# Kernel tuning notes

Hardware: AMD Instinct MI355X
Metric: run time of the kernel (lower is better)

## Reference

```python
import jax, jax.numpy as jnp
import numpy as np

B = 64; PAST = 128; FUTURE = 64; HID = 64; HEADS = 4
F = 16 + 8 + 24 + 3  # out_preprocess = 51


def _pre(cat, num, emb0, emb1, emb2):
    # pre_processing: embedding lookups per categorical column + last 3 float cols
    return jnp.concatenate([emb0[cat[:, 0]], emb1[cat[:, 1]], emb2[cat[:, 2]], num], axis=-1)


def _gat_conv(x, edge_index, lin_w, att_src, att_dst, bias, heads, out_ch):
    # PyG GATConv: concat=False (head mean), add_self_loops=True, leaky_relu slope 0.2
    N = x.shape[0]
    loops = jnp.arange(N, dtype=edge_index.dtype)
    src = jnp.concatenate([edge_index[0], loops])
    dst = jnp.concatenate([edge_index[1], loops])
    h = (x @ lin_w).reshape(N, heads, out_ch)          # [N, H, C]
    a_src = (h * att_src).sum(-1)                      # [N, H]
    a_dst = (h * att_dst).sum(-1)
    e = jax.nn.leaky_relu(a_src[src] + a_dst[dst], 0.2)  # [E, H]
    m = jax.lax.stop_gradient(jax.ops.segment_max(e, dst, num_segments=N))
    ex = jnp.exp(e - m[dst])
    s = jax.ops.segment_sum(ex, dst, num_segments=N)
    alpha = ex / (s[dst] + 1e-16)                      # softmax over in-edges per node
    out = jax.ops.segment_sum(alpha[:, :, None] * h[src], dst, num_segments=N)
    return out.mean(1) + bias                          # concat=False -> mean over heads


def setup_inputs() -> dict:
    ks = jax.random.split(jax.random.key(0), 17)
    N1, N2 = B * PAST, B * FUTURE
    E1, E2 = N1 * 16, N2 * 16
    return dict(
        cat1=jax.random.randint(ks[0], (N1, 3), 0, 7),
        num1=jax.random.normal(ks[1], (N1, 3), dtype=jnp.float32),
        cat2=jax.random.randint(ks[2], (N2, 3), 0, 7),
        num2=jax.random.normal(ks[3], (N2, 3), dtype=jnp.float32),
        e1=jax.random.randint(ks[4], (2, E1), 0, N1),
        e2=jax.random.randint(ks[5], (2, E2), 0, N2),
        A=jax.random.randint(ks[6], (PAST + FUTURE, PAST + FUTURE), 0, 2),
        emb0=0.1 * jax.random.normal(ks[7], (24, 16), dtype=jnp.float32),
        emb1=0.1 * jax.random.normal(ks[8], (7, 8), dtype=jnp.float32),
        emb2=0.1 * jax.random.normal(ks[9], (500, 24), dtype=jnp.float32),
        g1_lin=0.1 * jax.random.normal(ks[10], (F, HEADS * (F - 1)), dtype=jnp.float32),
        g1_asrc=0.1 * jax.random.normal(ks[11], (HEADS, F - 1), dtype=jnp.float32),
        g1_adst=0.1 * jax.random.normal(ks[12], (HEADS, F - 1), dtype=jnp.float32),
        g1_b=jnp.zeros((F - 1,), dtype=jnp.float32),
        g2_lin=0.1 * jax.random.normal(ks[13], (F, HEADS), dtype=jnp.float32),
        g2_asrc=0.1 * jax.random.normal(ks[14], (HEADS, 1), dtype=jnp.float32),
        g2_adst=0.1 * jax.random.normal(ks[15], (HEADS, 1), dtype=jnp.float32),
        g2_b=jnp.zeros((1,), dtype=jnp.float32),
        W=0.1 * jax.random.normal(ks[16], (F - 1, HID), dtype=jnp.float32),
    )


def reference(cat1, num1, cat2, num2, e1, e2, A, emb0, emb1, emb2,
              g1_lin, g1_asrc, g1_adst, g1_b, g2_lin, g2_asrc, g2_adst, g2_b, W):
    x = _pre(cat1, num1, emb0, emb1, emb2)                       # [B*PAST, F]
    x2 = _pre(cat2, num2, emb0, emb1, emb2).reshape(B, FUTURE, F)
    x1 = _gat_conv(x, e1, g1_lin, g1_asrc, g1_adst, g1_b, HEADS, F - 1).reshape(B, PAST, F - 1)
    # pairwise diff between every (future, past) node pair within a graph
    diff = x1[:, None, :, :] - x2[:, :, None, :F - 1]            # [B, FUTURE, PAST, F-1]
    M = W @ W.T
    M = M + M.T                                                  # WW^T + (WW^T)^T
    # original builds full [PAST, PAST] quadratic form and extracts diagonal;
    # compute only the diagonal: -0.5 * diff_i M diff_i
    alpha = -0.5 * jnp.einsum('bfpd,de,bfpe->bfp', diff, M, diff)
    mask = A[:PAST, PAST:].T                                     # [FUTURE, PAST]
    alpha = jnp.where(mask == 0, -jnp.inf, alpha)
    alpha = jax.nn.softmax(alpha, axis=-1)
    y_past = x.reshape(B, PAST, F)[:, :, -1:]                    # [B, PAST, 1]
    tmp = alpha @ y_past                                         # [B, FUTURE, 1]
    x2b = jnp.concatenate([x2[:, :, :F - 1], tmp], axis=-1)
    out = _gat_conv(x2b.reshape(-1, F), e2, g2_lin, g2_asrc, g2_adst, g2_b, HEADS, 1)
    return out.reshape(B, FUTURE)
```

## Files before the change

kernel.cpp:

```cpp
#include <hip/hip_runtime.h>

static constexpr int B_ = 64, PAST = 128, FUTURE = 64, F_ = 51;
static constexpr int N1 = B_ * PAST;
static constexpr int N2 = B_ * FUTURE;
static constexpr int E1 = N1 * 16;
static constexpr int E2 = N2 * 16;
static constexpr int MAXDEG = 64;
static constexpr int PB = 512;
static constexpr int FB = 256;
static constexpr int XITEMS = E1 + N1 + E2 + N2 + FUTURE * PAST;
static constexpr int XB = XITEMS / 256;
static constexpr int POISON_I = (int)0xAAAAAAAA;

__device__ __forceinline__ int depoison(int v) {
    int d = v - POISON_I;
    return (d >= 0 && d < 1000000) ? d : v;
}

__device__ __forceinline__
float node_feat(const int* cat, const float* num, const float* e0, const float* e1,
                const float* e2, int n, int t) {
    if (t < 16) return e0[cat[n * 3 + 0] * 16 + t];
    if (t < 24) return e1[cat[n * 3 + 1] * 8 + (t - 16)];
    if (t < 48) return e2[cat[n * 3 + 2] * 24 + (t - 24)];
    return num[n * 3 + (t - 48)];
}

__global__ __launch_bounds__(256) void k_all(
        const int* __restrict__ cat1, const float* __restrict__ num1,
        const int* __restrict__ cat2, const float* __restrict__ num2,
        const int* __restrict__ e1, const int* __restrict__ e2,
        const int* __restrict__ A,
        const float* __restrict__ emb0, const float* __restrict__ emb1,
        const float* __restrict__ emb2,
        const float* __restrict__ g1_lin, const float* __restrict__ g1_asrc,
        const float* __restrict__ g1_adst, const float* __restrict__ W,
        float* __restrict__ h1, float* __restrict__ asrc1, float* __restrict__ adst1,
        float* __restrict__ y1, float* __restrict__ x2g, float* __restrict__ P2,
        int* __restrict__ count1, int* __restrict__ slot1,
        int* __restrict__ count2, int* __restrict__ slot2,
        int* __restrict__ maskT) {
    __shared__ float L[10704];
    int blk = blockIdx.x, t = threadIdx.x;
    int lane = t & 63, wv = t >> 6;

    if (blk < PB) {
        float* Lg = L;
        float* Lx = L + 10200;
        float* redS = L + 10252;
        float* redD = L + 10452;
        for (int i = t; i < 10200; i += 256) Lg[i] = g1_lin[i];
        int n0 = blk * 16;
        for (int ni = 0; ni < 16; ++ni) {
            int n = n0 + ni;
            __syncthreads();
            if (t < F_) {
                float xv = node_feat(cat1, num1, emb0, emb1, emb2, n, t);
                Lx[t] = xv;
                if (t == 50) y1[n] = xv;
            }
            __syncthreads();
            if (t < 200) {
                float acc = 0.f;
                #pragma unroll
                for (int j = 0; j < F_; ++j) acc += Lx[j] * Lg[j * 200 + t];
                h1[n * 200 + t] = acc;
                redS[t] = acc * g1_asrc[t];
                redD[t] = acc * g1_adst[t];
            }
            __syncthreads();
            float s = (lane < 50) ? redS[wv * 50 + lane] : 0.f;
            float d = (lane < 50) ? redD[wv * 50 + lane] : 0.f;
            #pragma unroll
            for (int m = 32; m >= 1; m >>= 1) {
                s += __shfl_xor(s, m);
                d += __shfl_xor(d, m);
            }
            if (lane == 0) {
                asrc1[n * 4 + wv] = s;
                adst1[n * 4 + wv] = d;
            }
        }
        return;
    }

    if (blk < PB + FB) {
        float* Lw = L;
        float* Lx = L + 3200;
        for (int i = t; i < 3200; i += 256) Lw[i] = W[i];
        int n0 = (blk - PB) * 16;
        for (int r = 0; r < 4; ++r) {
            __syncthreads();
            if (t < 204) {
                int which = t / 51, j = t - which * 51;
                int n = n0 + r * 4 + which;
                float xv = node_feat(cat2, num2, emb0, emb1, emb2, n, j);
                Lx[which * 51 + j] = xv;
                x2g[n * F_ + j] = xv;
            }
            __syncthreads();
            int sub = t >> 6, k = t & 63;
            int n = n0 + r * 4 + sub;
            float acc = 0.f;
            #pragma unroll
            for (int j = 0; j < 50; ++j) acc += Lx[sub * 51 + j] * Lw[j * 64 + k];
            P2[n * 64 + k] = acc;
        }
        return;
    }

    int i = (blk - PB - FB) * 256 + t;
    if (i < E1) {
        int src = e1[i], dst = e1[E1 + i];
        int pos = depoison(atomicAdd(&count1[dst], 1));
        if (pos < MAXDEG) slot1[dst * MAXDEG + pos] = src;
    } else if (i < E1 + N1) {
        int n = i - E1;
        int pos = depoison(atomicAdd(&count1[n], 1));
        if (pos < MAXDEG) slot1[n * MAXDEG + pos] = n;
    } else if (i < E1 + N1 + E2) {
        int k = i - E1 - N1;
        int src = e2[k], dst = e2[E2 + k];
        int pos = depoison(atomicAdd(&count2[dst], 1));
        if (pos < MAXDEG) slot2[dst * MAXDEG + pos] = src;
    } else if (i < E1 + N1 + E2 + N2) {
        int n = i - E1 - N1 - E2;
        int pos = depoison(atomicAdd(&count2[n], 1));
        if (pos < MAXDEG) slot2[n * MAXDEG + pos] = n;
    } else {
        int k = i - (E1 + N1 + E2 + N2);
        int f = k >> 7, pp = k & 127;
        maskT[k] = A[pp * 192 + PAST + f];
    }
}

__global__ __launch_bounds__(256) void k_gat1(
        const int* __restrict__ count1, const int* __restrict__ slot1,
        const float* __restrict__ h1, const float* __restrict__ asrc1,
        const float* __restrict__ adst1, const float* __restrict__ g1_b,
        const float* __restrict__ W, float* __restrict__ P1) {
    __shared__ int   Ssrc[4][64];
    __shared__ float Sw[4][4][64];
    __shared__ float Sx[4][64];
    int t = threadIdx.x, lane = t & 63, wv = t >> 6;
    int n = (blockIdx.x * 256 + t) >> 6;
    int deg = min(depoison(count1[n]), MAXDEG);
    int my_src = (lane < deg) ? slot1[n * MAXDEG + lane] : 0;
    float ad0 = adst1[n * 4 + 0], ad1 = adst1[n * 4 + 1];
    float ad2 = adst1[n * 4 + 2], ad3 = adst1[n * 4 + 3];
    float ex0 = 0.f, ex1 = 0.f, ex2 = 0.f, ex3 = 0.f;
    if (lane < deg) {
        float e0 = asrc1[my_src * 4 + 0] + ad0;
        float e1 = asrc1[my_src * 4 + 1] + ad1;
        float e2 = asrc1[my_src * 4 + 2] + ad2;
        float e3 = asrc1[my_src * 4 + 3] + ad3;
        e0 = e0 >= 0.f ? e0 : 0.2f * e0;  ex0 = __expf(e0);
        e1 = e1 >= 0.f ? e1 : 0.2f * e1;  ex1 = __expf(e1);
        e2 = e2 >= 0.f ? e2 : 0.2f * e2;  ex2 = __expf(e2);
        e3 = e3 >= 0.f ? e3 : 0.2f * e3;  ex3 = __expf(e3);
    }
    float s0 = ex0, s1 = ex1, s2 = ex2, s3 = ex3;
    #pragma unroll
    for (int m = 32; m >= 1; m >>= 1) {
        s0 += __shfl_xor(s0, m);
        s1 += __shfl_xor(s1, m);
        s2 += __shfl_xor(s2, m);
        s3 += __shfl_xor(s3, m);
    }
    Ssrc[wv][lane] = my_src;
    Sw[wv][0][lane] = ex0 / (s0 + 1e-16f);
    Sw[wv][1][lane] = ex1 / (s1 + 1e-16f);
    Sw[wv][2][lane] = ex2 / (s2 + 1e-16f);
    Sw[wv][3][lane] = ex3 / (s3 + 1e-16f);
    __syncthreads();
    float acc0 = 0.f, acc1 = 0.f, acc2 = 0.f, acc3 = 0.f;
    for (int i = 0; i < deg; ++i) {
        int srci = Ssrc[wv][i];
        float w0 = Sw[wv][0][i], w1 = Sw[wv][1][i];
        float w2 = Sw[wv][2][i], w3 = Sw[wv][3][i];
        if (lane < 50) {
            const float* hr = &h1[srci * 200];
            acc0 += w0 * hr[lane];
            acc1 += w1 * hr[50 + lane];
            acc2 += w2 * hr[100 + lane];
            acc3 += w3 * hr[150 + lane];
        }
    }
    if (lane < 50)
        Sx[wv][lane] = 0.25f * (acc0 + acc1 + acc2 + acc3) + g1_b[lane];
    __syncthreads();
    float a = 0.f;
    #pragma unroll
    for (int j = 0; j < 50; ++j) a += Sx[wv][j] * W[j * 64 + lane];
    P1[n * 64 + lane] = a;
}

__global__ __launch_bounds__(256) void k_attn(
        const float* __restrict__ P1, const float* __restrict__ P2,
        const int* __restrict__ maskT, const float* __restrict__ y1,
        const float* __restrict__ x2g, const float* __restrict__ g2_lin,
        float* __restrict__ h2g) {
    __shared__ float P1s[64 * 129];
    __shared__ float ys[128];
    int b = blockIdx.x >> 2, fg = blockIdx.x & 3;
    int t = threadIdx.x, lane = t & 63, wv = t >> 6;
    const float* P1b = P1 + b * 8192;
    for (int i = t; i < 8192; i += 256) {
        int pp = i >> 6, kk = i & 63;
        P1s[kk * 129 + pp] = P1b[i];
    }
    if (t < 128) ys[t] = y1[b * 128 + t];
    __syncthreads();
    for (int j = 0; j < 4; ++j) {
        int f = fg * 16 + wv * 4 + j;
        int q = b * 64 + f;
        float p2k = P2[q * 64 + lane];
        float d2a = 0.f, d2b = 0.f;
        for (int k = 0; k < 64; ++k) {
            float bk = __shfl(p2k, k);
            float va = P1s[k * 129 + lane] - bk;
            float vb = P1s[k * 129 + 64 + lane] - bk;
            d2a += va * va;
            d2b += vb * vb;
        }
        int ma = maskT[f * 128 + lane];
        int mb = maskT[f * 128 + 64 + lane];
        float va = ma ? -d2a : -1e30f;
        float vb = mb ? -d2b : -1e30f;
        float mx = fmaxf(va, vb);
        #pragma unroll
        for (int m = 32; m >= 1; m >>= 1) mx = fmaxf(mx, __shfl_xor(mx, m));
        float wa = ma ? __expf(va - mx) : 0.f;
        float wb = mb ? __expf(vb - mx) : 0.f;
        float sw = wa + wb;
        float sy = wa * ys[lane] + wb * ys[64 + lane];
        #pragma unroll
        for (int m = 32; m >= 1; m >>= 1) {
            sw += __shfl_xor(sw, m);
            sy += __shfl_xor(sy, m);
        }
        float tsh = sy / sw;
        float xv = (lane < 50) ? x2g[q * F_ + lane] : 0.f;
        #pragma unroll
        for (int h = 0; h < 4; ++h) {
            float c = xv * g2_lin[lane * 4 + h];
            #pragma unroll
            for (int m = 32; m >= 1; m >>= 1) c += __shfl_xor(c, m);
            c += tsh * g2_lin[50 * 4 + h];
            if (lane == h) h2g[q * 4 + h] = c;
        }
    }
}

__global__ __launch_bounds__(256) void k_gat2(
        const int* __restrict__ count2, const int* __restrict__ slot2,
        const float* __restrict__ h2g, const float* __restrict__ g2_asrc,
        const float* __restrict__ g2_adst, const float* __restrict__ g2_b,
        float* __restrict__ out) {
    int wave = (blockIdx.x * blockDim.x + threadIdx.x) >> 6;
    int lane = threadIdx.x & 63;
    if (wave >= N2) return;
    int n = wave;
    int deg = min(depoison(count2[n]), MAXDEG);
    int my_src = (lane < deg) ? slot2[n * MAXDEG + lane] : 0;
    float ex[4], nm[4], adterm[4], as[4];
    #pragma unroll
    for (int h = 0; h < 4; ++h) {
        as[h] = g2_asrc[h];
        adterm[h] = h2g[n * 4 + h] * g2_adst[h];
        ex[h] = 0.f; nm[h] = 0.f;
    }
    if (lane < deg) {
        #pragma unroll
        for (int h = 0; h < 4; ++h) {
            float hs = h2g[my_src * 4 + h];
            float e = hs * as[h] + adterm[h];
            e = e >= 0.f ? e : 0.2f * e;
            float xv = __expf(e);
            ex[h] = xv;
            nm[h] = xv * hs;
        }
    }
    #pragma unroll
    for (int m = 32; m >= 1; m >>= 1) {
        #pragma unroll
        for (int h = 0; h < 4; ++h) {
            ex[h] += __shfl_xor(ex[h], m);
            nm[h] += __shfl_xor(nm[h], m);
        }
    }
    if (lane == 0) {
        float o = 0.f;
        #pragma unroll
        for (int h = 0; h < 4; ++h) o += nm[h] / (ex[h] + 1e-16f);
        out[n] = 0.25f * o + g2_b[0];
    }
}

extern "C" void kernel_launch(void* const* d_in, const int* in_sizes, int n_in,
                              void* d_out, int out_size, void* d_ws, size_t ws_size,
                              hipStream_t stream) {
    const int*   cat1    = (const int*)  d_in[0];
    const float* num1    = (const float*)d_in[1];
    const int*   cat2    = (const int*)  d_in[2];
    const float* num2    = (const float*)d_in[3];
    const int*   e1      = (const int*)  d_in[4];
    const int*   e2      = (const int*)  d_in[5];
    const int*   A       = (const int*)  d_in[6];
    const float* emb0    = (const float*)d_in[7];
    const float* emb1    = (const float*)d_in[8];
    const float* emb2    = (const float*)d_in[9];
    const float* g1_lin  = (const float*)d_in[10];
    const float* g1_asrc = (const float*)d_in[11];
    const float* g1_adst = (const float*)d_in[12];
    const float* g1_b    = (const float*)d_in[13];
    const float* g2_lin  = (const float*)d_in[14];
    const float* g2_asrc = (const float*)d_in[15];
    const float* g2_adst = (const float*)d_in[16];
    const float* g2_b    = (const float*)d_in[17];
    const float* W       = (const float*)d_in[18];
    float* out = (float*)d_out;

    int*   count1 = (int*)d_ws;
    int*   count2 = count1 + N1;
    int*   slot1  = count2 + N2;
    int*   slot2  = slot1 + N1 * MAXDEG;
    int*   maskT  = slot2 + N2 * MAXDEG;
    float* h1     = (float*)(maskT + FUTURE * PAST);
    float* asrc1  = h1 + N1 * 200;
    float* adst1  = asrc1 + N1 * 4;
    float* y1     = adst1 + N1 * 4;
    float* x2g    = y1 + N1;
    float* P1     = x2g + N2 * F_;
    float* P2     = P1 + N1 * 64;
    float* h2g    = P2 + N2 * 64;

    k_all<<<PB + FB + XB, 256, 0, stream>>>(cat1, num1, cat2, num2, e1, e2, A,
                                            emb0, emb1, emb2, g1_lin, g1_asrc, g1_adst, W,
                                            h1, asrc1, adst1, y1, x2g, P2,
                                            count1, slot1, count2, slot2, maskT);
    k_gat1<<<N1 / 4, 256, 0, stream>>>(count1, slot1, h1, asrc1, adst1, g1_b, W, P1);
    k_attn<<<B_ * 4, 256, 0, stream>>>(P1, P2, maskT, y1, x2g, g2_lin, h2g);
    k_gat2<<<N2 / 4, 256, 0, stream>>>(count2, slot2, h2g, g2_asrc, g2_adst, g2_b, out);
}
```

Before: 160.9 us.

## Map one node per wave in prep kernel and double attention grid

The prep kernel used to stage the 10K-float g1_lin matrix in shared memory and loop over 16 nodes per block with three barriers per node. It now assigns one node per wavefront, broadcasts features with shuffles, reads weights straight from global/L2, and splits the per-head attention dot products across lanes with shuffle reductions. The aim is to drop the shared-memory staging, the barriers and the long serial per-block loop, in exchange for more blocks and repeated global weight reads. The attention kernel also launches twice as many blocks, each handling half as many future rows, which raises occupancy but makes each block reload the same P1 tile.

```diff
diff --git a/kernel.cpp b/kernel.cpp
--- a/kernel.cpp
+++ b/kernel.cpp
@@ -6,10 +6,10 @@
 static constexpr int E1 = N1 * 16;
 static constexpr int E2 = N2 * 16;
 static constexpr int MAXDEG = 64;
-static constexpr int PB = 512;
-static constexpr int FB = 256;
 static constexpr int XITEMS = E1 + N1 + E2 + N2 + FUTURE * PAST;
-static constexpr int XB = XITEMS / 256;
+static constexpr int PASTB = N1 / 4;
+static constexpr int FUTB  = N2 / 4;
+static constexpr int XB    = XITEMS / 256;
 static constexpr int POISON_I = (int)0xAAAAAAAA;
 
 __device__ __forceinline__ int depoison(int v) {
@@ -26,7 +26,7 @@
     return num[n * 3 + (t - 48)];
 }
 
-__global__ __launch_bounds__(256) void k_all(
+__global__ __launch_bounds__(256) void k_prep(
         const int* __restrict__ cat1, const float* __restrict__ num1,
         const int* __restrict__ cat2, const float* __restrict__ num2,
         const int* __restrict__ e1, const int* __restrict__ e2,
@@ -40,76 +40,67 @@
         int* __restrict__ count1, int* __restrict__ slot1,
         int* __restrict__ count2, int* __restrict__ slot2,
         int* __restrict__ maskT) {
-    __shared__ float L[10704];
     int blk = blockIdx.x, t = threadIdx.x;
     int lane = t & 63, wv = t >> 6;
 
-    if (blk < PB) {
-        float* Lg = L;
-        float* Lx = L + 10200;
-        float* redS = L + 10252;
-        float* redD = L + 10452;
-        for (int i = t; i < 10200; i += 256) Lg[i] = g1_lin[i];
-        int n0 = blk * 16;
-        for (int ni = 0; ni < 16; ++ni) {
-            int n = n0 + ni;
-            __syncthreads();
-            if (t < F_) {
-                float xv = node_feat(cat1, num1, emb0, emb1, emb2, n, t);
-                Lx[t] = xv;
-                if (t == 50) y1[n] = xv;
-            }
-            __syncthreads();
-            if (t < 200) {
-                float acc = 0.f;
-                #pragma unroll
-                for (int j = 0; j < F_; ++j) acc += Lx[j] * Lg[j * 200 + t];
-                h1[n * 200 + t] = acc;
-                redS[t] = acc * g1_asrc[t];
-                redD[t] = acc * g1_adst[t];
-            }
-            __syncthreads();
-            float s = (lane < 50) ? redS[wv * 50 + lane] : 0.f;
-            float d = (lane < 50) ? redD[wv * 50 + lane] : 0.f;
-            #pragma unroll
-            for (int m = 32; m >= 1; m >>= 1) {
-                s += __shfl_xor(s, m);
-                d += __shfl_xor(d, m);
-            }
-            if (lane == 0) {
-                asrc1[n * 4 + wv] = s;
-                adst1[n * 4 + wv] = d;
-            }
+    if (blk < PASTB) {
+        int n = blk * 4 + wv;
+        float xv = (lane < F_) ? node_feat(cat1, num1, emb0, emb1, emb2, n, lane) : 0.f;
+        if (lane == 50) y1[n] = xv;
+        float acc0 = 0.f, acc1 = 0.f, acc2 = 0.f, acc3 = 0.f;
+        #pragma unroll
+        for (int j = 0; j < F_; ++j) {
+            float xj = __shfl(xv, j);
+            const float* g = g1_lin + j * 200;
+            acc0 += xj * g[lane];
+            acc1 += xj * g[64 + lane];
+            acc2 += xj * g[128 + lane];
+            if (lane < 8) acc3 += xj * g[192 + lane];
+        }
+        float* hr = h1 + n * 200;
+        hr[lane] = acc0; hr[64 + lane] = acc1; hr[128 + lane] = acc2;
+        if (lane < 8) hr[192 + lane] = acc3;
+        float ga0 = g1_asrc[lane], ga1 = g1_asrc[64 + lane], ga2 = g1_asrc[128 + lane];
+        float gd0 = g1_adst[lane], gd1 = g1_adst[64 + lane], gd2 = g1_adst[128 + lane];
+        float ga3 = (lane < 8) ? g1_asrc[192 + lane] : 0.f;
+        float gd3 = (lane < 8) ? g1_adst[192 + lane] : 0.f;
+        float s0 = (lane < 50) ? acc0 * ga0 : 0.f;
+        float s1 = ((lane >= 50) ? acc0 * ga0 : 0.f) + ((lane < 36) ? acc1 * ga1 : 0.f);
+        float s2 = ((lane >= 36) ? acc1 * ga1 : 0.f) + ((lane < 22) ? acc2 * ga2 : 0.f);
+        float s3 = ((lane >= 22) ? acc2 * ga2 : 0.f) + ((lane < 8) ? acc3 * ga3 : 0.f);
+        float d0 = (lane < 50) ? acc0 * gd0 : 0.f;
+        float d1 = ((lane >= 50) ? acc0 * gd0 : 0.f) + ((lane < 36) ? acc1 * gd1 : 0.f);
+        float d2 = ((lane >= 36) ? acc1 * gd1 : 0.f) + ((lane < 22) ? acc2 * gd2 : 0.f);
+        float d3 = ((lane >= 22) ? acc2 * gd2 : 0.f) + ((lane < 8) ? acc3 * gd3 : 0.f);
+        #pragma unroll
+        for (int m = 32; m >= 1; m >>= 1) {
+            s0 += __shfl_xor(s0, m); s1 += __shfl_xor(s1, m);
+            s2 += __shfl_xor(s2, m); s3 += __shfl_xor(s3, m);
+            d0 += __shfl_xor(d0, m); d1 += __shfl_xor(d1, m);
+            d2 += __shfl_xor(d2, m); d3 += __shfl_xor(d3, m);
+        }
+        if (lane < 8) {
+            int h = lane & 3;
+            float vS = (h == 0) ? s0 : (h == 1) ? s1 : (h == 2) ? s2 : s3;
+            float vD = (h == 0) ? d0 : (h == 1) ? d1 : (h == 2) ? d2 : d3;
+            if (lane < 4) asrc1[n * 4 + h] = vS;
+            else          adst1[n * 4 + h] = vD;
         }
         return;
     }
 
-    if (blk < PB + FB) {
-        float* Lw = L;
-        float* Lx = L + 3200;
-        for (int i = t; i < 3200; i += 256) Lw[i] = W[i];
-        int n0 = (blk - PB) * 16;
-        for (int r = 0; r < 4; ++r) {
-            __syncthreads();
-            if (t < 204) {
-                int which = t / 51, j = t - which * 51;
-                int n = n0 + r * 4 + which;
-                float xv = node_feat(cat2, num2, emb0, emb1, emb2, n, j);
-                Lx[which * 51 + j] = xv;
-                x2g[n * F_ + j] = xv;
-            }
-            __syncthreads();
-            int sub = t >> 6, k = t & 63;
-            int n = n0 + r * 4 + sub;
-            float acc = 0.f;
-            #pragma unroll
-            for (int j = 0; j < 50; ++j) acc += Lx[sub * 51 + j] * Lw[j * 64 + k];
-            P2[n * 64 + k] = acc;
-        }
+    if (blk < PASTB + FUTB) {
+        int n = (blk - PASTB) * 4 + wv;
+        float xv = (lane < F_) ? node_feat(cat2, num2, emb0, emb1, emb2, n, lane) : 0.f;
+        if (lane < F_) x2g[n * F_ + lane] = xv;
+        float acc = 0.f;
+        #pragma unroll
+        for (int j = 0; j < 50; ++j) acc += __shfl(xv, j) * W[j * 64 + lane];
+        P2[n * 64 + lane] = acc;
         return;
     }
 
-    int i = (blk - PB - FB) * 256 + t;
+    int i = (blk - PASTB - FUTB) * 256 + t;
     if (i < E1) {
         int src = e1[i], dst = e1[E1 + i];
         int pos = depoison(atomicAdd(&count1[dst], 1));
@@ -202,7 +193,7 @@
         float* __restrict__ h2g) {
     __shared__ float P1s[64 * 129];
     __shared__ float ys[128];
-    int b = blockIdx.x >> 2, fg = blockIdx.x & 3;
+    int b = blockIdx.x >> 3, fg = blockIdx.x & 7;
     int t = threadIdx.x, lane = t & 63, wv = t >> 6;
     const float* P1b = P1 + b * 8192;
     for (int i = t; i < 8192; i += 256) {
@@ -211,8 +202,8 @@
     }
     if (t < 128) ys[t] = y1[b * 128 + t];
     __syncthreads();
-    for (int j = 0; j < 4; ++j) {
-        int f = fg * 16 + wv * 4 + j;
+    for (int j = 0; j < 2; ++j) {
+        int f = fg * 8 + wv * 2 + j;
         int q = b * 64 + f;
         float p2k = P2[q * 64 + lane];
         float d2a = 0.f, d2b = 0.f;
@@ -335,11 +326,12 @@
     float* P2     = P1 + N1 * 64;
     float* h2g    = P2 + N2 * 64;
 
-    k_all<<<PB + FB + XB, 256, 0, stream>>>(cat1, num1, cat2, num2, e1, e2, A,
-                                            emb0, emb1, emb2, g1_lin, g1_asrc, g1_adst, W,
-                                            h1, asrc1, adst1, y1, x2g, P2,
-                                            count1, slot1, count2, slot2, maskT);
+    k_prep<<<PASTB + FUTB + XB, 256, 0, stream>>>(cat1, num1, cat2, num2, e1, e2, A,
+                                                  emb0, emb1, emb2,
+                                                  g1_lin, g1_asrc, g1_adst, W,
+                                                  h1, asrc1, adst1, y1, x2g, P2,
+                                                  count1, slot1, count2, slot2, maskT);
     k_gat1<<<N1 / 4, 256, 0, stream>>>(count1, slot1, h1, asrc1, adst1, g1_b, W, P1);
-    k_attn<<<B_ * 4, 256, 0, stream>>>(P1, P2, maskT, y1, x2g, g2_lin, h2g);
+    k_attn<<<B_ * 8, 256, 0, stream>>>(P1, P2, maskT, y1, x2g, g2_lin, h2g);
     k_gat2<<<N2 / 4, 256, 0, stream>>>(count2, slot2, h2g, g2_asrc, g2_adst, g2_b, out);
 }
```

Result: slower. 181.1 us (+12.5%).
